# Optimization experiments

Hardware: AMD Instinct MI355X
Metric: run time of the kernel (lower is better)

The kernel has to match this reference:

```python
import jax, jax.numpy as jnp
import numpy as np

K = 4  # number of neighbors, per kNN-VC convention

def setup_inputs() -> dict:
    key = jax.random.key(0)
    k1, k2 = jax.random.split(key)
    source_feats = jax.random.normal(k1, (2048, 1024), dtype=jnp.float32)
    target_feats = jax.random.normal(k2, (50000, 1024), dtype=jnp.float32)
    return {"source_feats": source_feats, "target_feats": target_feats}

def reference(source_feats, target_feats):
    # cosine kNN matching: for each source frame, find K nearest target frames
    # under cosine distance (= highest cosine similarity), then average them.
    eps = jnp.asarray(1e-8, source_feats.dtype)
    src_n = source_feats / jnp.maximum(jnp.linalg.norm(source_feats, axis=-1, keepdims=True), eps)
    tgt_n = target_feats / jnp.maximum(jnp.linalg.norm(target_feats, axis=-1, keepdims=True), eps)
    # [T_src, T_tgt] cosine similarity
    sims = jnp.einsum('sd,td->st', src_n, tgt_n)
    _, idx = jax.lax.top_k(sims, K)          # [T_src, K]
    neighbors = target_feats[idx]             # [T_src, K, D]
    out = jnp.mean(neighbors, axis=1)         # [T_src, D]
    return out
```

## Files before the change

### kernel.cpp

```cpp
#include <hip/hip_runtime.h>
#include <math.h>

#define S_ROWS 2048
#define T_ROWS 50000
#define DIM    1024
#define KNN    4

#define BM 128
#define BN 128
#define KSL 64
#define NSLAB (DIM / KSL)
#define NBUF 3
#define TILES_PER_CHUNK 4
#define CHUNK_COLS (BN * TILES_PER_CHUNK)
#define NUM_CHUNKS ((T_ROWS + CHUNK_COLS - 1) / CHUNK_COLS)
#define T_PAD (NUM_CHUNKS * CHUNK_COLS)
#define NCAND (NUM_CHUNKS * KNN)
#define REFINE 16
#define SP 67
#define QSCALE 500.0f

typedef unsigned int uint;
typedef unsigned long long u64;
typedef signed char i8;
typedef __attribute__((ext_vector_type(4))) int i32x4;

__device__ __forceinline__ u64 packI(int v, int idx) {
  return ((u64)((uint)v ^ 0x80000000u) << 32) | (uint)(~idx);
}

template <int N>
__device__ __forceinline__ void insU(u64 p, u64 (&tv)[N]) {
  if (p <= tv[N - 1]) return;
  tv[N - 1] = p;
#pragma unroll
  for (int j = N - 1; j > 0; --j) {
    if (tv[j] > tv[j - 1]) { u64 t = tv[j]; tv[j] = tv[j - 1]; tv[j - 1] = t; }
  }
}

__device__ __forceinline__ void llds16(const void* g, void* l) {
  __builtin_amdgcn_global_load_lds(
      reinterpret_cast<__attribute__((address_space(1))) void*>(
          reinterpret_cast<uintptr_t>(g)),
      reinterpret_cast<__attribute__((address_space(3))) void*>(
          (unsigned)reinterpret_cast<uintptr_t>(l)),
      16, 0, 0);
}

__device__ __forceinline__ int imax2(int a, int b) { return a > b ? a : b; }

__global__ __launch_bounds__(256) void quant_kernel(const float* __restrict__ in,
                                                    i8* __restrict__ outq, int nvalid) {
  const int row = blockIdx.x;
  const int tid = threadIdx.x;
  if (row >= nvalid) {
    ((uint*)(outq + ((size_t)row << 10)))[tid] = 0u;
    return;
  }
  __shared__ float red[4];
  float4 v = ((const float4*)(in + ((size_t)row << 10)))[tid];
  float s = v.x * v.x + v.y * v.y + v.z * v.z + v.w * v.w;
#pragma unroll
  for (int off = 32; off; off >>= 1) s += __shfl_down(s, off, 64);
  if ((tid & 63) == 0) red[tid >> 6] = s;
  __syncthreads();
  float tot = red[0] + red[1] + red[2] + red[3];
  float r = QSCALE / fmaxf(sqrtf(tot), 1e-8f);
  int q0 = __float2int_rn(v.x * r), q1 = __float2int_rn(v.y * r);
  int q2 = __float2int_rn(v.z * r), q3 = __float2int_rn(v.w * r);
  q0 = imax2(-127, (q0 < 127 ? q0 : 127));
  q1 = imax2(-127, (q1 < 127 ? q1 : 127));
  q2 = imax2(-127, (q2 < 127 ? q2 : 127));
  q3 = imax2(-127, (q3 < 127 ? q3 : 127));
  uint packed = ((uint)q0 & 255u) | (((uint)q1 & 255u) << 8) |
                (((uint)q2 & 255u) << 16) | (((uint)q3 & 255u) << 24);
  ((uint*)(outq + ((size_t)row << 10)))[tid] = packed;
}

union __align__(16) SimSmem {
  i8 ab[NBUF][2 * BM * KSL];
  int sims[BM * SP];
  u64 mb[256 * KNN];
};

__device__ __forceinline__ void stage64(const i8* aP, const i8* bP, i8* aL, i8* bL) {
  llds16(aP, aL);
  llds16(aP + 16384, aL + 1024);
  llds16(bP, bL);
  llds16(bP + 16384, bL + 1024);
}

__global__ __launch_bounds__(256) void sim_i8_kernel(const i8* __restrict__ srcq,
                                                     const i8* __restrict__ tgtq,
                                                     u64* __restrict__ partials) {
  __shared__ SimSmem sm;

  const int tid = threadIdx.x;
  const int lane = tid & 63;
  const int wave = tid >> 6;
  const int qr = (wave >> 1) * 64;
  const int qch = wave & 1;
  const int m = lane & 15;
  const int quad = lane >> 4;
  const int r0 = blockIdx.x * BM;
  const int chunk = blockIdx.y;

  const int srow4 = lane >> 2;
  const int scb4 = (lane & 3) ^ (srow4 & 3);
  const i8* aLane = srcq + (((size_t)(r0 + wave * 32 + srow4)) << 10) + scb4 * 16;

  const int swz = (quad ^ (m & 3)) << 4;
  const int aoff0 = ((qr + m) << 6) + swz;
  const int boff0 = ((qch * 64 + m) << 6) + swz;

  u64 topp[KNN] = {0, 0, 0, 0};
  int thrI = (int)0x80000000;

  for (int tile = 0; tile < TILES_PER_CHUNK; ++tile) {
    const int c0 = chunk * CHUNK_COLS + tile * BN;
    const i8* bLane = tgtq + (((size_t)(c0 + wave * 32 + srow4)) << 10) + scb4 * 16;

    i32x4 acc[4][4];
#pragma unroll
    for (int i = 0; i < 4; ++i)
#pragma unroll
      for (int j = 0; j < 4; ++j) acc[i][j] = (i32x4){0, 0, 0, 0};

    stage64(aLane, bLane, sm.ab[0] + wave * 2048, sm.ab[0] + 8192 + wave * 2048);
    stage64(aLane + 64, bLane + 64, sm.ab[1] + wave * 2048, sm.ab[1] + 8192 + wave * 2048);

#pragma unroll
    for (int k = 0; k < NSLAB; ++k) {
      if (k == NSLAB - 1)
        asm volatile("s_waitcnt vmcnt(0)" ::: "memory");
      else
        asm volatile("s_waitcnt vmcnt(4)" ::: "memory");
      asm volatile("s_waitcnt lgkmcnt(0)" ::: "memory");
      __builtin_amdgcn_s_barrier();
      __builtin_amdgcn_sched_barrier(0);

      const i8* base = sm.ab[k % NBUF];
      i32x4 af[4], bf[4];
#pragma unroll
      for (int i = 0; i < 4; ++i) af[i] = *(const i32x4*)(base + aoff0 + i * 1024);
#pragma unroll
      for (int j = 0; j < 4; ++j) bf[j] = *(const i32x4*)(base + 8192 + boff0 + j * 1024);

      if (k + 2 < NSLAB) {
        i8* nb = sm.ab[(k + 2) % NBUF];
        stage64(aLane + ((k + 2) << 6), bLane + ((k + 2) << 6),
                nb + wave * 2048, nb + 8192 + wave * 2048);
      }

      __builtin_amdgcn_s_setprio(1);
#pragma unroll
      for (int i = 0; i < 4; ++i)
#pragma unroll
        for (int j = 0; j < 4; ++j)
          acc[i][j] = __builtin_amdgcn_mfma_i32_16x16x64_i8(af[i], bf[j], acc[i][j], 0, 0, 0);
      __builtin_amdgcn_s_setprio(0);
    }

    __syncthreads();

#pragma unroll
    for (int ph = 0; ph < 2; ++ph) {
      if (qch == ph) {
#pragma unroll
        for (int i = 0; i < 4; ++i)
#pragma unroll
          for (int j = 0; j < 4; ++j)
#pragma unroll
            for (int reg = 0; reg < 4; ++reg)
              sm.sims[(qr + i * 16 + quad * 4 + reg) * SP + j * 16 + m] = acc[i][j][reg];
      }
      __syncthreads();
      {
        const int rowl = tid & 127;
        const int chh = tid >> 7;
        const int* srow = &sm.sims[rowl * SP + chh * 32];
        const int gbase = c0 + ph * 64 + chh * 32;
#pragma unroll
        for (int c = 0; c < 32; c += 4) {
          int a = srow[c], b = srow[c + 1], d2 = srow[c + 2], e = srow[c + 3];
          int mx = imax2(imax2(a, b), imax2(d2, e));
          if (mx > thrI) {
            const int g = gbase + c;
            if (g + 0 < T_ROWS) insU<KNN>(packI(a, g + 0), topp);
            if (g + 1 < T_ROWS) insU<KNN>(packI(b, g + 1), topp);
            if (g + 2 < T_ROWS) insU<KNN>(packI(d2, g + 2), topp);
            if (g + 3 < T_ROWS) insU<KNN>(packI(e, g + 3), topp);
            thrI = (int)((uint)(topp[KNN - 1] >> 32) ^ 0x80000000u);
          }
        }
      }
      __syncthreads();
    }
  }

#pragma unroll
  for (int j = 0; j < KNN; ++j) sm.mb[tid * KNN + j] = topp[j];
  __syncthreads();
  if (tid < 128) {
#pragma unroll
    for (int j = 0; j < KNN; ++j) insU<KNN>(sm.mb[(tid + 128) * KNN + j], topp);
    u64* dst = partials + ((size_t)(r0 + tid) * NUM_CHUNKS + chunk) * KNN;
#pragma unroll
    for (int j = 0; j < KNN; ++j) dst[j] = topp[j];
  }
}

__global__ __launch_bounds__(256) void merge_gather_kernel(
    const u64* __restrict__ partials, const float* __restrict__ src,
    const float* __restrict__ tgt, float* __restrict__ out) {
  const int row = blockIdx.x;
  const int tid = threadIdx.x;
  const int lane = tid & 63;
  const int wave = tid >> 6;
  __shared__ u64 cbuf[NCAND];
  __shared__ u64 part8[8][REFINE];
  __shared__ int cand[REFINE];
  __shared__ double cval[REFINE];
  __shared__ int fin[KNN];

  for (int c = tid; c < NCAND; c += 256) cbuf[c] = partials[(size_t)row * NCAND + c];
  __syncthreads();

  if (tid < 8) {
    u64 t16[REFINE];
#pragma unroll
    for (int j = 0; j < REFINE; ++j) t16[j] = 0;
    const int base = tid * (NCAND / 8);
    for (int c = 0; c < NCAND / 8; ++c) insU<REFINE>(cbuf[base + c], t16);
#pragma unroll
    for (int j = 0; j < REFINE; ++j) part8[tid][j] = t16[j];
  }
  __syncthreads();
  if (tid == 0) {
    u64 t16[REFINE];
#pragma unroll
    for (int j = 0; j < REFINE; ++j) t16[j] = 0;
    for (int s = 0; s < 8; ++s)
#pragma unroll
      for (int j = 0; j < REFINE; ++j) insU<REFINE>(part8[s][j], t16);
#pragma unroll
    for (int j = 0; j < REFINE; ++j) cand[j] = (int)(~(uint)t16[j]);
  }
  __syncthreads();

  const float4* s4 = (const float4*)(src + ((size_t)row << 10));
  float4 s0 = s4[lane], s1 = s4[lane + 64], s2 = s4[lane + 128], s3 = s4[lane + 192];
  double ss = (double)s0.x * s0.x + (double)s0.y * s0.y + (double)s0.z * s0.z + (double)s0.w * s0.w
            + (double)s1.x * s1.x + (double)s1.y * s1.y + (double)s1.z * s1.z + (double)s1.w * s1.w
            + (double)s2.x * s2.x + (double)s2.y * s2.y + (double)s2.z * s2.z + (double)s2.w * s2.w
            + (double)s3.x * s3.x + (double)s3.y * s3.y + (double)s3.z * s3.z + (double)s3.w * s3.w;
#pragma unroll
  for (int off = 32; off; off >>= 1) ss += __shfl_down(ss, off, 64);
  ss = __shfl(ss, 0, 64);
  const double sn = fmax(sqrt(ss), 1e-8);

  for (int cc = wave; cc < REFINE; cc += 4) {
    const float4* t4 = (const float4*)(tgt + ((size_t)cand[cc] << 10));
    float4 t0 = t4[lane], t1 = t4[lane + 64], t2 = t4[lane + 128], t3 = t4[lane + 192];
    double dd = (double)s0.x * t0.x + (double)s0.y * t0.y + (double)s0.z * t0.z + (double)s0.w * t0.w
              + (double)s1.x * t1.x + (double)s1.y * t1.y + (double)s1.z * t1.z + (double)s1.w * t1.w
              + (double)s2.x * t2.x + (double)s2.y * t2.y + (double)s2.z * t2.z + (double)s2.w * t2.w
              + (double)s3.x * t3.x + (double)s3.y * t3.y + (double)s3.z * t3.z + (double)s3.w * t3.w;
    double tt = (double)t0.x * t0.x + (double)t0.y * t0.y + (double)t0.z * t0.z + (double)t0.w * t0.w
              + (double)t1.x * t1.x + (double)t1.y * t1.y + (double)t1.z * t1.z + (double)t1.w * t1.w
              + (double)t2.x * t2.x + (double)t2.y * t2.y + (double)t2.z * t2.z + (double)t2.w * t2.w
              + (double)t3.x * t3.x + (double)t3.y * t3.y + (double)t3.z * t3.z + (double)t3.w * t3.w;
#pragma unroll
    for (int off = 32; off; off >>= 1) {
      dd += __shfl_down(dd, off, 64);
      tt += __shfl_down(tt, off, 64);
    }
    if (lane == 0) cval[cc] = dd / (sn * fmax(sqrt(tt), 1e-8));
  }
  __syncthreads();

  if (tid == 0) {
    bool used[REFINE];
#pragma unroll
    for (int j = 0; j < REFINE; ++j) used[j] = false;
    for (int k = 0; k < KNN; ++k) {
      int bj = -1; double bv = 0.0; int bidx = 0x7fffffff;
      for (int j = 0; j < REFINE; ++j) {
        if (used[j]) continue;
        if (bj < 0 || cval[j] > bv || (cval[j] == bv && cand[j] < bidx)) {
          bj = j; bv = cval[j]; bidx = cand[j];
        }
      }
      used[bj] = true;
      fin[k] = cand[bj];
    }
  }
  __syncthreads();

  const int d = tid * 4;
  float4 a = *(const float4*)(tgt + ((size_t)fin[0] << 10) + d);
  float4 b = *(const float4*)(tgt + ((size_t)fin[1] << 10) + d);
  float4 c = *(const float4*)(tgt + ((size_t)fin[2] << 10) + d);
  float4 e = *(const float4*)(tgt + ((size_t)fin[3] << 10) + d);
  float4 o;
  o.x = 0.25f * (a.x + b.x + c.x + e.x);
  o.y = 0.25f * (a.y + b.y + c.y + e.y);
  o.z = 0.25f * (a.z + b.z + c.z + e.z);
  o.w = 0.25f * (a.w + b.w + c.w + e.w);
  *(float4*)(out + ((size_t)row << 10) + d) = o;
}

extern "C" void kernel_launch(void* const* d_in, const int* in_sizes, int n_in,
                              void* d_out, int out_size, void* d_ws, size_t ws_size,
                              hipStream_t stream) {
  const float* src = (const float*)d_in[0];
  const float* tgt = (const float*)d_in[1];
  float* out = (float*)d_out;
  char* ws = (char*)d_ws;

  const size_t SRCQ_B = (size_t)S_ROWS << 10;
  const size_t TGTQ_B = (size_t)T_PAD << 10;

  i8* srcq = (i8*)ws;
  i8* tgtq = (i8*)(ws + SRCQ_B);
  u64* partials = (u64*)(ws + SRCQ_B + TGTQ_B);

  quant_kernel<<<S_ROWS, 256, 0, stream>>>(src, srcq, S_ROWS);
  quant_kernel<<<T_PAD, 256, 0, stream>>>(tgt, tgtq, T_ROWS);

  dim3 g3(S_ROWS / BM, NUM_CHUNKS);
  sim_i8_kernel<<<g3, 256, 0, stream>>>(srcq, tgtq, partials);

  merge_gather_kernel<<<S_ROWS, 256, 0, stream>>>(partials, src, tgt, out);
}
```

Baseline: 631.6 us.

## Enlarge similarity GEMM tile to 256x256 with 512-thread blocks

Raises the int8 similarity block tile from 128x128 to 256x256 and runs it with 8 waves of 512 threads, each wave owning a 128x64 sub-tile. Half the waves stage A and half stage B. The K pipeline drops from triple to double buffering and waits for all loads at every slab. The epilogue now runs in 8 phases with a narrower sims buffer, and two threads per row share the top-k scan, followed by a pairwise merge. The aim is more MFMA work per LDS byte and less global traffic per output. The cost is higher register pressure, fewer chunks in flight, and less overlap of loads with compute.

```diff
diff --git a/kernel.cpp b/kernel.cpp
--- a/kernel.cpp
+++ b/kernel.cpp
@@ -6,18 +6,18 @@
 #define DIM    1024
 #define KNN    4
 
-#define BM 128
-#define BN 128
+#define BM 256
+#define BN 256
 #define KSL 64
 #define NSLAB (DIM / KSL)
-#define NBUF 3
-#define TILES_PER_CHUNK 4
+#define NBUF 2
+#define TILES_PER_CHUNK 2
 #define CHUNK_COLS (BN * TILES_PER_CHUNK)
 #define NUM_CHUNKS ((T_ROWS + CHUNK_COLS - 1) / CHUNK_COLS)
 #define T_PAD (NUM_CHUNKS * CHUNK_COLS)
 #define NCAND (NUM_CHUNKS * KNN)
 #define REFINE 16
-#define SP 67
+#define SP2 36
 #define QSCALE 500.0f
 
 typedef unsigned int uint;
@@ -79,28 +79,21 @@
 }
 
 union __align__(16) SimSmem {
-  i8 ab[NBUF][2 * BM * KSL];
-  int sims[BM * SP];
-  u64 mb[256 * KNN];
+  i8 ab[NBUF][BM * KSL + BN * KSL];
+  int sims[BM * SP2];
+  u64 mb[512 * KNN];
 };
 
-__device__ __forceinline__ void stage64(const i8* aP, const i8* bP, i8* aL, i8* bL) {
-  llds16(aP, aL);
-  llds16(aP + 16384, aL + 1024);
-  llds16(bP, bL);
-  llds16(bP + 16384, bL + 1024);
-}
-
-__global__ __launch_bounds__(256) void sim_i8_kernel(const i8* __restrict__ srcq,
-                                                     const i8* __restrict__ tgtq,
-                                                     u64* __restrict__ partials) {
+__global__ __launch_bounds__(512, 2) void sim_i8_kernel(const i8* __restrict__ srcq,
+                                                        const i8* __restrict__ tgtq,
+                                                        u64* __restrict__ partials) {
   __shared__ SimSmem sm;
 
   const int tid = threadIdx.x;
   const int lane = tid & 63;
   const int wave = tid >> 6;
-  const int qr = (wave >> 1) * 64;
-  const int qch = wave & 1;
+  const int wr = wave >> 2;
+  const int wc = wave & 3;
   const int m = lane & 15;
   const int quad = lane >> 4;
   const int r0 = blockIdx.x * BM;
@@ -108,89 +101,100 @@
 
   const int srow4 = lane >> 2;
   const int scb4 = (lane & 3) ^ (srow4 & 3);
-  const i8* aLane = srcq + (((size_t)(r0 + wave * 32 + srow4)) << 10) + scb4 * 16;
+  const bool stA = wave < 4;
+  const int sw = stA ? wave : wave - 4;
+  const i8* aStage = srcq + (((size_t)(r0 + sw * 64 + srow4)) << 10) + scb4 * 16;
+  const int ldsOff = (stA ? 0 : BM * KSL) + sw * 4096;
 
   const int swz = (quad ^ (m & 3)) << 4;
-  const int aoff0 = ((qr + m) << 6) + swz;
-  const int boff0 = ((qch * 64 + m) << 6) + swz;
+  const int aoff0 = ((wr * 128 + m) << 6) + swz;
+  const int boff0 = BM * KSL + ((wc * 64 + m) << 6) + swz;
 
   u64 topp[KNN] = {0, 0, 0, 0};
   int thrI = (int)0x80000000;
 
+#pragma unroll 1
   for (int tile = 0; tile < TILES_PER_CHUNK; ++tile) {
     const int c0 = chunk * CHUNK_COLS + tile * BN;
-    const i8* bLane = tgtq + (((size_t)(c0 + wave * 32 + srow4)) << 10) + scb4 * 16;
-
-    i32x4 acc[4][4];
-#pragma unroll
-    for (int i = 0; i < 4; ++i)
+    const i8* gBase = stA ? aStage
+                          : tgtq + (((size_t)(c0 + sw * 64 + srow4)) << 10) + scb4 * 16;
+
+    i32x4 acc[8][4];
+#pragma unroll
+    for (int i = 0; i < 8; ++i)
 #pragma unroll
       for (int j = 0; j < 4; ++j) acc[i][j] = (i32x4){0, 0, 0, 0};
 
-    stage64(aLane, bLane, sm.ab[0] + wave * 2048, sm.ab[0] + 8192 + wave * 2048);
-    stage64(aLane + 64, bLane + 64, sm.ab[1] + wave * 2048, sm.ab[1] + 8192 + wave * 2048);
+    {
+      i8* lp = sm.ab[0] + ldsOff;
+      llds16(gBase, lp);
+      llds16(gBase + 16384, lp + 1024);
+      llds16(gBase + 32768, lp + 2048);
+      llds16(gBase + 49152, lp + 3072);
+    }
 
 #pragma unroll
     for (int k = 0; k < NSLAB; ++k) {
-      if (k == NSLAB - 1)
-        asm volatile("s_waitcnt vmcnt(0)" ::: "memory");
-      else
-        asm volatile("s_waitcnt vmcnt(4)" ::: "memory");
+      asm volatile("s_waitcnt vmcnt(0)" ::: "memory");
       asm volatile("s_waitcnt lgkmcnt(0)" ::: "memory");
       __builtin_amdgcn_s_barrier();
       __builtin_amdgcn_sched_barrier(0);
 
-      const i8* base = sm.ab[k % NBUF];
-      i32x4 af[4], bf[4];
-#pragma unroll
-      for (int i = 0; i < 4; ++i) af[i] = *(const i32x4*)(base + aoff0 + i * 1024);
-#pragma unroll
-      for (int j = 0; j < 4; ++j) bf[j] = *(const i32x4*)(base + 8192 + boff0 + j * 1024);
-
-      if (k + 2 < NSLAB) {
-        i8* nb = sm.ab[(k + 2) % NBUF];
-        stage64(aLane + ((k + 2) << 6), bLane + ((k + 2) << 6),
-                nb + wave * 2048, nb + 8192 + wave * 2048);
+      const i8* base = sm.ab[k & 1];
+      i32x4 af[8], bf[4];
+#pragma unroll
+      for (int i = 0; i < 8; ++i) af[i] = *(const i32x4*)(base + aoff0 + i * 1024);
+#pragma unroll
+      for (int j = 0; j < 4; ++j) bf[j] = *(const i32x4*)(base + boff0 + j * 1024);
+
+      if (k + 1 < NSLAB) {
+        const i8* gp = gBase + ((k + 1) << 6);
+        i8* lp = sm.ab[(k + 1) & 1] + ldsOff;
+        llds16(gp, lp);
+        llds16(gp + 16384, lp + 1024);
+        llds16(gp + 32768, lp + 2048);
+        llds16(gp + 49152, lp + 3072);
       }
 
       __builtin_amdgcn_s_setprio(1);
 #pragma unroll
-      for (int i = 0; i < 4; ++i)
+      for (int i = 0; i < 8; ++i)
 #pragma unroll
         for (int j = 0; j < 4; ++j)
           acc[i][j] = __builtin_amdgcn_mfma_i32_16x16x64_i8(af[i], bf[j], acc[i][j], 0, 0, 0);
       __builtin_amdgcn_s_setprio(0);
     }
-
     __syncthreads();
 
-#pragma unroll
-    for (int ph = 0; ph < 2; ++ph) {
-      if (qch == ph) {
-#pragma unroll
-        for (int i = 0; i < 4; ++i)
-#pragma unroll
-          for (int j = 0; j < 4; ++j)
+#pragma unroll 1
+    for (int ph = 0; ph < 8; ++ph) {
+      if (wc == (ph >> 1)) {
+        const int jj = ph & 1;
+#pragma unroll
+        for (int i = 0; i < 8; ++i)
+#pragma unroll
+          for (int j2 = 0; j2 < 2; ++j2)
 #pragma unroll
             for (int reg = 0; reg < 4; ++reg)
-              sm.sims[(qr + i * 16 + quad * 4 + reg) * SP + j * 16 + m] = acc[i][j][reg];
+              sm.sims[(wr * 128 + i * 16 + quad * 4 + reg) * SP2 + j2 * 16 + m] =
+                  acc[i][jj * 2 + j2][reg];
       }
       __syncthreads();
       {
-        const int rowl = tid & 127;
-        const int chh = tid >> 7;
-        const int* srow = &sm.sims[rowl * SP + chh * 32];
-        const int gbase = c0 + ph * 64 + chh * 32;
-#pragma unroll
-        for (int c = 0; c < 32; c += 4) {
-          int a = srow[c], b = srow[c + 1], d2 = srow[c + 2], e = srow[c + 3];
-          int mx = imax2(imax2(a, b), imax2(d2, e));
+        const int rowl = tid >> 1;
+        const int chh = tid & 1;
+        const int* srow = &sm.sims[rowl * SP2 + chh * 16];
+        const int gbase = c0 + (ph >> 1) * 64 + (ph & 1) * 32 + chh * 16;
+#pragma unroll
+        for (int c = 0; c < 16; c += 4) {
+          i32x4 v = *(const i32x4*)(srow + c);
+          int mx = imax2(imax2(v[0], v[1]), imax2(v[2], v[3]));
           if (mx > thrI) {
             const int g = gbase + c;
-            if (g + 0 < T_ROWS) insU<KNN>(packI(a, g + 0), topp);
-            if (g + 1 < T_ROWS) insU<KNN>(packI(b, g + 1), topp);
-            if (g + 2 < T_ROWS) insU<KNN>(packI(d2, g + 2), topp);
-            if (g + 3 < T_ROWS) insU<KNN>(packI(e, g + 3), topp);
+            if (g + 0 < T_ROWS) insU<KNN>(packI(v[0], g + 0), topp);
+            if (g + 1 < T_ROWS) insU<KNN>(packI(v[1], g + 1), topp);
+            if (g + 2 < T_ROWS) insU<KNN>(packI(v[2], g + 2), topp);
+            if (g + 3 < T_ROWS) insU<KNN>(packI(v[3], g + 3), topp);
             thrI = (int)((uint)(topp[KNN - 1] >> 32) ^ 0x80000000u);
           }
         }
@@ -202,12 +206,15 @@
 #pragma unroll
   for (int j = 0; j < KNN; ++j) sm.mb[tid * KNN + j] = topp[j];
   __syncthreads();
-  if (tid < 128) {
-#pragma unroll
-    for (int j = 0; j < KNN; ++j) insU<KNN>(sm.mb[(tid + 128) * KNN + j], topp);
+  if (tid < BM) {
+    u64 tt[KNN];
+#pragma unroll
+    for (int j = 0; j < KNN; ++j) tt[j] = sm.mb[(2 * tid) * KNN + j];
+#pragma unroll
+    for (int j = 0; j < KNN; ++j) insU<KNN>(sm.mb[(2 * tid + 1) * KNN + j], tt);
     u64* dst = partials + ((size_t)(r0 + tid) * NUM_CHUNKS + chunk) * KNN;
 #pragma unroll
-    for (int j = 0; j < KNN; ++j) dst[j] = topp[j];
+    for (int j = 0; j < KNN; ++j) dst[j] = tt[j];
   }
 }
 
@@ -330,7 +337,7 @@
   quant_kernel<<<T_PAD, 256, 0, stream>>>(tgt, tgtq, T_ROWS);
 
   dim3 g3(S_ROWS / BM, NUM_CHUNKS);
-  sim_i8_kernel<<<g3, 256, 0, stream>>>(srcq, tgtq, partials);
+  sim_i8_kernel<<<g3, 512, 0, stream>>>(srcq, tgtq, partials);
 
   merge_gather_kernel<<<S_ROWS, 256, 0, stream>>>(partials, src, tgt, out);
 }
```

New measurement: 1.791 ms. +183.6%, slower.
